# Kernel optimization log

Hardware: AMD Instinct MI355X
Metric: run time of the kernel (lower is better)

The kernel has to match this reference:

```python
import jax, jax.numpy as jnp
import numpy as np

B, S, C = 2, 2048, 1536
HQ, HKV = 16, 4
DQK, DV = 128, 96
MAX_POS = 2048
CLIP = 5.0
EPS = 1e-5


def layer_norm(x, g, b):
    mu = jnp.mean(x, axis=-1, keepdims=True)
    var = jnp.mean(jnp.square(x - mu), axis=-1, keepdims=True)
    return (x - mu) * jax.lax.rsqrt(var + EPS) * g + b


def rms_bn(x, g, ms):
    # eval-mode EMA RMS batch-norm: per-channel running mean-square `ms`
    return x * jax.lax.rsqrt(ms + EPS) * g


def rope(x):
    # x: [B, S, H, C] with C even
    c = x.shape[-1]
    nf = c // 2
    s = x.shape[1]
    positions = jnp.arange(s, dtype=x.dtype)
    lin = jnp.arange(nf, dtype=x.dtype)
    end = max(MAX_POS - nf + 1.0, 1.0)
    geom = jnp.exp(jnp.linspace(0.0, jnp.log(jnp.asarray(end, dtype=x.dtype)), nf))
    inv_freq = 1.0 / (lin + geom)
    theta = positions[:, None] * inv_freq          # [S, nf]
    theta = jnp.repeat(theta, 2, axis=-1)[:, None, :]  # [S, 1, C]
    x_rot = jnp.stack([-x[..., 1::2], x[..., ::2]], axis=-1).reshape(x.shape)
    return x * jnp.cos(theta) + x_rot * jnp.sin(theta)


def setup_inputs() -> dict:
    key = jax.random.key(0)
    ks = jax.random.split(key, 8)
    d = {
        'x': jax.random.normal(ks[0], (B, S, C), dtype=jnp.float32),
        'bn1_g': jnp.ones((C,), jnp.float32),
        'bn1_ms': jnp.ones((C,), jnp.float32),
        'Wq': jax.random.normal(ks[1], (C, HQ * DQK), jnp.float32) * 0.02,
        'Wk': jax.random.normal(ks[2], (C, HKV * DQK), jnp.float32) * 0.02,
        'Wv': jax.random.normal(ks[3], (C, HKV * DV), jnp.float32) * 0.02,
        'qn_g': jnp.ones((DQK,), jnp.float32), 'qn_b': jnp.zeros((DQK,), jnp.float32),
        'kn_g': jnp.ones((DQK,), jnp.float32), 'kn_b': jnp.zeros((DQK,), jnp.float32),
        'vn_g': jnp.ones((DV,), jnp.float32), 'vn_b': jnp.zeros((DV,), jnp.float32),
        'Wo': jax.random.normal(ks[4], (HQ * DV, C), jnp.float32) * 0.02,
        'bo': jnp.zeros((C,), jnp.float32),
        'bn2_g': jnp.ones((C,), jnp.float32),
        'bn2_ms': jnp.ones((C,), jnp.float32),
    }
    return d


def reference(x, bn1_g, bn1_ms, Wq, Wk, Wv, qn_g, qn_b, kn_g, kn_b, vn_g, vn_b, Wo, bo, bn2_g, bn2_ms):
    rep = HQ // HKV
    h = rms_bn(x, bn1_g, bn1_ms)                       # [B,S,C]
    q = (h @ Wq).reshape(B, S, HQ, DQK)
    k = (h @ Wk).reshape(B, S, HKV, DQK)
    v = (h @ Wv).reshape(B, S, HKV, DV)
    q = layer_norm(q, qn_g, qn_b)
    k = layer_norm(k, kn_g, kn_b)
    v = layer_norm(v, vn_g, vn_b)
    q = rope(q)
    k = rope(k)
    # torch .repeat(1,1,rep,1) tiles head axis: [h0..hkv-1] * rep
    k = jnp.tile(k, (1, 1, rep, 1))                    # [B,S,HQ,DQK]
    v = jnp.tile(v, (1, 1, rep, 1))                    # [B,S,HQ,DV]
    logits = jnp.einsum('bshc,bShc->bhsS', q, k) / (DQK ** 0.5)
    logits = jnp.tanh(logits / CLIP) * CLIP
    attn = jax.nn.softmax(logits, axis=-1)
    y = jnp.einsum('bhsS,bShc->bshc', attn, v)         # [B,S,HQ,DV]
    y = y.reshape(B, S, HQ * DV)
    y = y @ Wo + bo
    y = rms_bn(y, bn2_g, bn2_ms)
    return y
```

## Files before the change

kernel.cpp:

```cpp
#include <hip/hip_runtime.h>
#include <hip/hip_bf16.h>
#include <math.h>

typedef __hip_bfloat16 bf16;
typedef __attribute__((ext_vector_type(8))) short short8;
typedef __attribute__((ext_vector_type(4))) short short4s;
typedef __attribute__((ext_vector_type(4))) float f32x4;

constexpr int Bb=2, Ss=2048, Cc=1536, HQn=16, HKVn=4, Dqk=128, Dv=96;
constexpr int NR   = Bb*Ss;
constexpr int NQKV = HQn*Dqk + HKVn*Dqk + HKVn*Dv;
constexpr int COL_K = HQn*Dqk;
constexpr int COL_V = COL_K + HKVn*Dqk;
constexpr int NY   = HQn*Dv;
constexpr float EPSf=1e-5f, CLIPf=5.0f;
constexpr float LOG2E = 1.44269504089f;

__device__ __forceinline__ float s2f(short s) {
    unsigned u = ((unsigned)(unsigned short)s) << 16;
    return __builtin_bit_cast(float, u);
}
__device__ __forceinline__ short f2s(float v) {
    bf16 b = __float2bfloat16(v);
    return __builtin_bit_cast(short, b);
}
__device__ __forceinline__ bool is_bf(const void* tagp) {
    return ((*(const unsigned*)tagp) & 0xFFFFu) != 0u;
}
__device__ __forceinline__ float ldd(const void* p, size_t i, bool bf) {
    return bf ? s2f(((const short*)p)[i]) : ((const float*)p)[i];
}

__global__ __launch_bounds__(256) void k_pre(const void* g1, const void* ms1,
        const void* bo, const void* g2, const void* ms2,
        float* __restrict__ ascale, float* __restrict__ ebias,
        float* __restrict__ escale, float2* __restrict__ tab) {
    bool bf = is_bf(ms1);
    int idx = blockIdx.x*256 + threadIdx.x;
    if (idx < Cc) {
        ascale[idx] = rsqrtf(ldd(ms1,idx,bf) + EPSf) * ldd(g1,idx,bf);
        ebias[idx]  = ldd(bo,idx,bf);
        escale[idx] = rsqrtf(ldd(ms2,idx,bf) + EPSf) * ldd(g2,idx,bf);
    }
    if (idx < Ss*64) {
        int s = idx >> 6, f = idx & 63;
        float geom = expf((float)f * (logf(1985.0f) * (1.0f/63.0f)));
        float invf = 1.0f / ((float)f + geom);
        float th = (float)s * invf;
        tab[idx] = make_float2(cosf(th), sinf(th));
    }
}

__global__ __launch_bounds__(256) void k_bn1(const void* __restrict__ x,
        const float* __restrict__ ascale, short* __restrict__ h, const void* tagp) {
    bool bf = is_bf(tagp);
    size_t i8 = (size_t)(blockIdx.x*256 + threadIdx.x) * 8;
    if (i8 >= (size_t)NR*Cc) return;
    int c = (int)(i8 % Cc);
    float xv[8];
    if (bf) {
        short8 xa = *(const short8*)((const short*)x + i8);
        #pragma unroll
        for (int j=0;j<8;++j) xv[j] = s2f(xa[j]);
    } else {
        const float* xf = (const float*)x + i8;
        #pragma unroll
        for (int j=0;j<8;++j) xv[j] = xf[j];
    }
    short8 o;
    #pragma unroll
    for (int j=0;j<8;++j) o[j] = f2s(xv[j] * ascale[c+j]);
    *(short8*)(h + i8) = o;
}

__global__ __launch_bounds__(256) void k_trw(const void* __restrict__ Wq,
        const void* __restrict__ Wk, const void* __restrict__ Wv,
        const void* __restrict__ Wo, short* __restrict__ WT, const void* tagp) {
    __shared__ short tile[32][33];
    bool bf = is_bf(tagp);
    int gt = blockIdx.x*32;
    int k0 = blockIdx.y*32;
    const void* W; int N, nl;
    if      (gt < 2048) { W = Wq; N = 2048; nl = gt; }
    else if (gt < 2560) { W = Wk; N = 512;  nl = gt - 2048; }
    else if (gt < 2944) { W = Wv; N = 384;  nl = gt - 2560; }
    else                { W = Wo; N = 1536; nl = gt - 2944; }
    int t = threadIdx.x, c = t & 31;
    #pragma unroll
    for (int r8=0; r8<32; r8+=8) {
        int r = r8 + (t>>5);
        tile[r][c] = f2s(ldd(W, (size_t)(k0+r)*N + nl + c, bf));
    }
    __syncthreads();
    #pragma unroll
    for (int r8=0; r8<32; r8+=8) {
        int r = r8 + (t>>5);
        WT[(size_t)(gt + r)*Cc + k0 + c] = tile[c][r];
    }
}

__global__ __launch_bounds__(256) void k_gemm(const short* __restrict__ A,
        const short* __restrict__ BT, void* __restrict__ Cout,
        int M, int N, int K,
        const float* __restrict__ ebias, const float* __restrict__ escale,
        int epi, const void* tagp) {
    __shared__ short As[128*32];
    __shared__ short Bs[128*32];
    const int t = threadIdx.x;
    const int w = t >> 6, lane = t & 63;
    const int l15 = lane & 15, quad = lane >> 4;
    const int wm = (w>>1)*64, wn = (w&1)*64;
    const int m0 = blockIdx.y*128, n0 = blockIdx.x*128;
    const int c0 = lane >> 2;
    const int koff = (lane & 3) * 8;

    f32x4 acc[4][4];
    #pragma unroll
    for (int i=0;i<4;++i)
        #pragma unroll
        for (int j=0;j<4;++j) acc[i][j] = (f32x4){0.f,0.f,0.f,0.f};

    for (int k0 = 0; k0 < K; k0 += 32) {
        __syncthreads();
        #pragma unroll
        for (int c=0; c<2; ++c) {
            int rA = w*32 + c*16;
            const short* ga = A  + (size_t)(m0 + rA + c0)*K + k0 + koff;
            const short* gb = BT + (size_t)(n0 + rA + c0)*K + k0 + koff;
            __builtin_amdgcn_global_load_lds(
                (const __attribute__((address_space(1))) void*)ga,
                (__attribute__((address_space(3))) void*)&As[rA*32], 16, 0, 0);
            __builtin_amdgcn_global_load_lds(
                (const __attribute__((address_space(1))) void*)gb,
                (__attribute__((address_space(3))) void*)&Bs[rA*32], 16, 0, 0);
        }
        __syncthreads();
        short8 af[4], bfr[4];
        #pragma unroll
        for (int mt=0; mt<4; ++mt)
            af[mt] = *(const short8*)&As[(wm + mt*16 + l15)*32 + quad*8];
        #pragma unroll
        for (int nt=0; nt<4; ++nt)
            bfr[nt] = *(const short8*)&Bs[(wn + nt*16 + l15)*32 + quad*8];
        #pragma unroll
        for (int mt=0; mt<4; ++mt)
            #pragma unroll
            for (int nt=0; nt<4; ++nt)
                acc[mt][nt] = __builtin_amdgcn_mfma_f32_16x16x32_bf16(
                    af[mt], bfr[nt], acc[mt][nt], 0, 0, 0);
    }

    const bool outf32 = epi && !is_bf(tagp);
    #pragma unroll
    for (int mt=0; mt<4; ++mt) {
        #pragma unroll
        for (int nt=0; nt<4; ++nt) {
            int col = n0 + wn + nt*16 + l15;
            float eb = epi ? ebias[col]  : 0.f;
            float es = epi ? escale[col] : 1.f;
            #pragma unroll
            for (int reg=0; reg<4; ++reg) {
                int row = m0 + wm + mt*16 + quad*4 + reg;
                float v = acc[mt][nt][reg];
                if (epi) v = (v + eb) * es;
                if (outf32) ((float*)Cout)[(size_t)row*N + col] = v;
                else        ((short*)Cout)[(size_t)row*N + col] = f2s(v);
            }
        }
    }
}

__global__ __launch_bounds__(256) void k_ln(short* __restrict__ qkvb,
        const float2* __restrict__ tab,
        const void* qg, const void* qb_, const void* kg, const void* kb_,
        const void* vg, const void* vb_, const void* tagp) {
    bool bf = is_bf(tagp);
    int R = blockIdx.x*4 + (threadIdx.x>>6);
    int lane = threadIdx.x & 63;
    int hidx = R % 24, bs = R / 24, s = bs % Ss;
    const void *g, *bia; int coff, D, dorope;
    if (hidx < 16)      { coff = hidx*Dqk;              D = Dqk; g = qg; bia = qb_; dorope = 1; }
    else if (hidx < 20) { coff = COL_K + (hidx-16)*Dqk; D = Dqk; g = kg; bia = kb_; dorope = 1; }
    else                { coff = COL_V + (hidx-20)*Dv;  D = Dv;  g = vg; bia = vb_; dorope = 0; }
    short* p = qkvb + (size_t)bs*NQKV + coff;
    int d0 = lane*2;
    bool act = d0 < D;
    float v0 = 0.f, v1 = 0.f;
    if (act) { v0 = s2f(p[d0]); v1 = s2f(p[d0+1]); }
    float sum = v0 + v1;
    #pragma unroll
    for (int m=1; m<64; m<<=1) sum += __shfl_xor(sum, m);
    float mu = sum / (float)D;
    float c0 = act ? v0-mu : 0.f, c1 = act ? v1-mu : 0.f;
    float sq = c0*c0 + c1*c1;
    #pragma unroll
    for (int m=1; m<64; m<<=1) sq += __shfl_xor(sq, m);
    float r = rsqrtf(sq/(float)D + EPSf);
    if (act) {
        float y0 = c0*r*ldd(g,d0,bf)   + ldd(bia,d0,bf);
        float y1 = c1*r*ldd(g,d0+1,bf) + ldd(bia,d0+1,bf);
        if (dorope) {
            float2 cs = tab[s*64 + lane];
            float t0 = y0*cs.x - y1*cs.y;
            y1 = y1*cs.x + y0*cs.y;
            y0 = t0;
        }
        p[d0] = f2s(y0); p[d0+1] = f2s(y1);
    }
}

__global__ __launch_bounds__(256) void k_trv(const short* __restrict__ qkvb,
        short* __restrict__ vT) {
    __shared__ short tile[32][33];
    int bs0 = blockIdx.x*32;
    int dg0 = blockIdx.y*32;
    int t = threadIdx.x, c = t & 31;
    #pragma unroll
    for (int r8=0; r8<32; r8+=8) {
        int r = r8 + (t>>5);
        tile[r][c] = qkvb[(size_t)(bs0+r)*NQKV + COL_V + dg0 + c];
    }
    __syncthreads();
    int b = bs0 >> 11, s0 = bs0 & 2047;
    #pragma unroll
    for (int r8=0; r8<32; r8+=8) {
        int r = r8 + (t>>5);
        vT[((size_t)(b*384 + dg0 + r))*Ss + s0 + c] = tile[c][r];
    }
}

__global__ __launch_bounds__(256) void k_attn(const short* __restrict__ qkvb,
        const short* __restrict__ vT, short* __restrict__ Yb) {
    __shared__ __align__(16) short Ks[64*136];
    __shared__ __align__(16) short VTs[96*72];
    __shared__ __align__(16) short Ps[128*72];
    const int q0 = blockIdx.x*128, hq = blockIdx.y, b = blockIdx.z;
    const int kvh = hq & (HKVn-1);
    const int t = threadIdx.x;
    const int w = t >> 6, lane = t & 63;
    const int l15 = lane & 15, quad = lane >> 4;
    const float ctan = 2.0f * (0.0883883476f / CLIPf) * LOG2E;
    const float c2   = -2.0f * CLIPf * LOG2E;

    short8 qf[2][4];
    #pragma unroll
    for (int qt=0; qt<2; ++qt) {
        const short* qp = qkvb + (size_t)(b*Ss + q0 + w*32 + qt*16 + l15)*NQKV + hq*Dqk;
        #pragma unroll
        for (int ds=0; ds<4; ++ds) qf[qt][ds] = *(const short8*)(qp + ds*32 + quad*8);
    }

    f32x4 oacc[2][6];
    #pragma unroll
    for (int qt=0; qt<2; ++qt)
        #pragma unroll
        for (int nt=0; nt<6; ++nt) oacc[qt][nt] = (f32x4){0.f,0.f,0.f,0.f};
    float lsum[2] = {0.f, 0.f};

    const short* Kb = qkvb + ((size_t)b*Ss)*NQKV + COL_K + kvh*Dqk;
    const short* Vb = vT + ((size_t)(b*HKVn + kvh)*Dv)*Ss;

    for (int kc = 0; kc < Ss/64; ++kc) {
        const int j0 = kc*64;
        __syncthreads();
        #pragma unroll
        for (int it=0; it<4; ++it) {
            int idx = it*256 + t;
            int key = idx >> 4, d = (idx & 15)*8;
            *(short8*)&Ks[key*136 + d] = *(const short8*)(Kb + (size_t)(j0+key)*NQKV + d);
        }
        #pragma unroll
        for (int it=0; it<3; ++it) {
            int idx = it*256 + t;
            int dv = idx >> 3, c8 = (idx & 7)*8;
            *(short8*)&VTs[dv*72 + c8] = *(const short8*)(Vb + (size_t)dv*Ss + j0 + c8);
        }
        __syncthreads();

        f32x4 sacc[4][2];
        #pragma unroll
        for (int kt=0; kt<4; ++kt)
            #pragma unroll
            for (int qt=0; qt<2; ++qt) sacc[kt][qt] = (f32x4){0.f,0.f,0.f,0.f};
        #pragma unroll
        for (int kt=0; kt<4; ++kt) {
            short8 kf[4];
            #pragma unroll
            for (int ds=0; ds<4; ++ds)
                kf[ds] = *(const short8*)&Ks[(kt*16 + l15)*136 + ds*32 + quad*8];
            #pragma unroll
            for (int qt=0; qt<2; ++qt)
                #pragma unroll
                for (int ds=0; ds<4; ++ds)
                    sacc[kt][qt] = __builtin_amdgcn_mfma_f32_16x16x32_bf16(
                        kf[ds], qf[qt][ds], sacc[kt][qt], 0, 0, 0);
        }

        #pragma unroll
        for (int kt=0; kt<4; ++kt)
            #pragma unroll
            for (int qt=0; qt<2; ++qt) {
                short4s pb;
                #pragma unroll
                for (int reg=0; reg<4; ++reg) {
                    float u = __builtin_amdgcn_exp2f(sacc[kt][qt][reg] * ctan);
                    float p = __builtin_amdgcn_exp2f(c2 * __builtin_amdgcn_rcpf(u + 1.0f));
                    short pb16 = f2s(p);
                    pb[reg] = pb16;
                    lsum[qt] += s2f(pb16);
                }
                *(short4s*)&Ps[(w*32 + qt*16 + l15)*72 + kt*16 + quad*4] = pb;
            }

        short8 vf[6][2];
        #pragma unroll
        for (int nt=0; nt<6; ++nt)
            #pragma unroll
            for (int ks=0; ks<2; ++ks)
                vf[nt][ks] = *(const short8*)&VTs[(nt*16 + l15)*72 + ks*32 + quad*8];
        #pragma unroll
        for (int qt=0; qt<2; ++qt) {
            short8 pf0 = *(const short8*)&Ps[(w*32 + qt*16 + l15)*72 + quad*8];
            short8 pf1 = *(const short8*)&Ps[(w*32 + qt*16 + l15)*72 + 32 + quad*8];
            #pragma unroll
            for (int nt=0; nt<6; ++nt) {
                oacc[qt][nt] = __builtin_amdgcn_mfma_f32_16x16x32_bf16(
                    pf0, vf[nt][0], oacc[qt][nt], 0, 0, 0);
                oacc[qt][nt] = __builtin_amdgcn_mfma_f32_16x16x32_bf16(
                    pf1, vf[nt][1], oacc[qt][nt], 0, 0, 0);
            }
        }
    }

    float lred[2];
    #pragma unroll
    for (int qt=0; qt<2; ++qt) {
        float l = lsum[qt];
        l += __shfl_xor(l, 16);
        l += __shfl_xor(l, 32);
        lred[qt] = l;
    }
    #pragma unroll
    for (int qt=0; qt<2; ++qt) {
        float rinv[4];
        #pragma unroll
        for (int reg=0; reg<4; ++reg)
            rinv[reg] = __builtin_amdgcn_rcpf(__shfl(lred[qt], quad*4 + reg, 16));
        #pragma unroll
        for (int nt=0; nt<6; ++nt)
            #pragma unroll
            for (int reg=0; reg<4; ++reg) {
                int row = q0 + w*32 + qt*16 + quad*4 + reg;
                Yb[(size_t)(b*Ss + row)*NY + hq*Dv + nt*16 + l15] =
                    f2s(oacc[qt][nt][reg] * rinv[reg]);
            }
    }
}

extern "C" void kernel_launch(void* const* d_in, const int* in_sizes, int n_in,
                              void* d_out, int out_size, void* d_ws, size_t ws_size,
                              hipStream_t stream) {
    const void* x     = d_in[0];
    const void* bn1g  = d_in[1];
    const void* bn1ms = d_in[2];
    const void* Wq    = d_in[3];
    const void* Wk    = d_in[4];
    const void* Wv    = d_in[5];
    const void* qng   = d_in[6];
    const void* qnb   = d_in[7];
    const void* kng   = d_in[8];
    const void* knb   = d_in[9];
    const void* vng   = d_in[10];
    const void* vnb   = d_in[11];
    const void* Wo    = d_in[12];
    const void* bo    = d_in[13];
    const void* bn2g  = d_in[14];
    const void* bn2ms = d_in[15];

    char* wsb = (char*)d_ws;
    float*  ascale = (float*)(wsb);
    float*  ebias  = (float*)(wsb + 6144);
    float*  escale = (float*)(wsb + 12288);
    float2* tab    = (float2*)(wsb + 18432);
    short*  h      = (short*)(wsb + 1067520);
    short*  WT     = (short*)(wsb + 13650432);
    short*  qkv    = (short*)(wsb + 27412992);
    short*  vT     = (short*)(wsb + 51530240);
    short*  y      = (short*)(wsb + 54675968);
    short*  WoT    = WT + (size_t)NQKV*Cc;

    k_pre<<<512, 256, 0, stream>>>(bn1g, bn1ms, bo, bn2g, bn2ms,
                                   ascale, ebias, escale, tab);
    k_bn1<<<(NR*Cc/8 + 255)/256, 256, 0, stream>>>(x, ascale, h, bn1ms);
    k_trw<<<dim3(4480/32, Cc/32), 256, 0, stream>>>(Wq, Wk, Wv, Wo, WT, bn1ms);

    k_gemm<<<dim3(NQKV/128, NR/128), 256, 0, stream>>>(
        h, WT, qkv, NR, NQKV, Cc, nullptr, nullptr, 0, bn1ms);

    k_ln<<<NR*24/4, 256, 0, stream>>>(qkv, tab, qng, qnb, kng, knb, vng, vnb, bn1ms);
    k_trv<<<dim3(NR/32, 384/32), 256, 0, stream>>>(qkv, vT);

    k_attn<<<dim3(Ss/128, HQn, Bb), 256, 0, stream>>>(qkv, vT, y);

    k_gemm<<<dim3(Cc/128, NR/128), 256, 0, stream>>>(
        y, WoT, d_out, NR, Cc, NY, ebias, escale, 1, bn1ms);
}
```

Baseline: 393.9 us.

## Fuse Q layernorm+RoPE into attention, shuffle P via bpermute, shrink attn blocks

Moves the Q-head LayerNorm and RoPE into the attention kernel's Q-fragment load, so k_ln now processes only K and V heads. P is no longer staged through shared memory; the bf16 probabilities are packed into registers and redistributed across lanes with ds_bpermute to form the A operand of the PV MFMA. Attention blocks shrink to 64 queries and 128 threads with a 3-blocks-per-CU launch bound, and the bn1 scale is computed inline in k_bn1 instead of being precomputed. Together these cut an elementwise pass and LDS traffic, at the cost of redoing the Q normalization work inside attention, more bpermute instructions, and K/V tiles being loaded into LDS twice as many times in total.

```diff
diff --git a/kernel.cpp b/kernel.cpp
--- a/kernel.cpp
+++ b/kernel.cpp
@@ -4,7 +4,7 @@
 
 typedef __hip_bfloat16 bf16;
 typedef __attribute__((ext_vector_type(8))) short short8;
-typedef __attribute__((ext_vector_type(4))) short short4s;
+typedef __attribute__((ext_vector_type(4))) int   int4v;
 typedef __attribute__((ext_vector_type(4))) float f32x4;
 
 constexpr int Bb=2, Ss=2048, Cc=1536, HQn=16, HKVn=4, Dqk=128, Dv=96;
@@ -31,14 +31,13 @@
     return bf ? s2f(((const short*)p)[i]) : ((const float*)p)[i];
 }
 
-__global__ __launch_bounds__(256) void k_pre(const void* g1, const void* ms1,
-        const void* bo, const void* g2, const void* ms2,
-        float* __restrict__ ascale, float* __restrict__ ebias,
-        float* __restrict__ escale, float2* __restrict__ tab) {
-    bool bf = is_bf(ms1);
+__global__ __launch_bounds__(256) void k_pre(const void* bo, const void* g2,
+        const void* ms2, const void* tagp,
+        float* __restrict__ ebias, float* __restrict__ escale,
+        float2* __restrict__ tab) {
+    bool bf = is_bf(tagp);
     int idx = blockIdx.x*256 + threadIdx.x;
     if (idx < Cc) {
-        ascale[idx] = rsqrtf(ldd(ms1,idx,bf) + EPSf) * ldd(g1,idx,bf);
         ebias[idx]  = ldd(bo,idx,bf);
         escale[idx] = rsqrtf(ldd(ms2,idx,bf) + EPSf) * ldd(g2,idx,bf);
     }
@@ -52,7 +51,8 @@
 }
 
 __global__ __launch_bounds__(256) void k_bn1(const void* __restrict__ x,
-        const float* __restrict__ ascale, short* __restrict__ h, const void* tagp) {
+        const void* __restrict__ g1, const void* __restrict__ ms1,
+        short* __restrict__ h, const void* tagp) {
     bool bf = is_bf(tagp);
     size_t i8 = (size_t)(blockIdx.x*256 + threadIdx.x) * 8;
     if (i8 >= (size_t)NR*Cc) return;
@@ -69,7 +69,10 @@
     }
     short8 o;
     #pragma unroll
-    for (int j=0;j<8;++j) o[j] = f2s(xv[j] * ascale[c+j]);
+    for (int j=0;j<8;++j) {
+        float sc = rsqrtf(ldd(ms1,c+j,bf) + EPSf) * ldd(g1,c+j,bf);
+        o[j] = f2s(xv[j] * sc);
+    }
     *(short8*)(h + i8) = o;
 }
 
@@ -172,16 +175,15 @@
 
 __global__ __launch_bounds__(256) void k_ln(short* __restrict__ qkvb,
         const float2* __restrict__ tab,
-        const void* qg, const void* qb_, const void* kg, const void* kb_,
-        const void* vg, const void* vb_, const void* tagp) {
+        const void* kg, const void* kb_, const void* vg, const void* vb_,
+        const void* tagp) {
     bool bf = is_bf(tagp);
     int R = blockIdx.x*4 + (threadIdx.x>>6);
     int lane = threadIdx.x & 63;
-    int hidx = R % 24, bs = R / 24, s = bs % Ss;
+    int hidx = R & 7, bs = R >> 3, s = bs & (Ss-1);
     const void *g, *bia; int coff, D, dorope;
-    if (hidx < 16)      { coff = hidx*Dqk;              D = Dqk; g = qg; bia = qb_; dorope = 1; }
-    else if (hidx < 20) { coff = COL_K + (hidx-16)*Dqk; D = Dqk; g = kg; bia = kb_; dorope = 1; }
-    else                { coff = COL_V + (hidx-20)*Dv;  D = Dv;  g = vg; bia = vb_; dorope = 0; }
+    if (hidx < 4) { coff = COL_K + hidx*Dqk;     D = Dqk; g = kg; bia = kb_; dorope = 1; }
+    else          { coff = COL_V + (hidx-4)*Dv;  D = Dv;  g = vg; bia = vb_; dorope = 0; }
     short* p = qkvb + (size_t)bs*NQKV + coff;
     int d0 = lane*2;
     bool act = d0 < D;
@@ -229,25 +231,62 @@
     }
 }
 
-__global__ __launch_bounds__(256) void k_attn(const short* __restrict__ qkvb,
-        const short* __restrict__ vT, short* __restrict__ Yb) {
+constexpr int QB = 64;
+__global__ __launch_bounds__(128, 3) void k_attn(const short* __restrict__ qkvb,
+        const short* __restrict__ vT, short* __restrict__ Yb,
+        const float2* __restrict__ tab, const void* __restrict__ qg,
+        const void* __restrict__ qb_, const void* tagp) {
     __shared__ __align__(16) short Ks[64*136];
     __shared__ __align__(16) short VTs[96*72];
-    __shared__ __align__(16) short Ps[128*72];
-    const int q0 = blockIdx.x*128, hq = blockIdx.y, b = blockIdx.z;
+    const int q0 = blockIdx.x*QB, hq = blockIdx.y, b = blockIdx.z;
     const int kvh = hq & (HKVn-1);
     const int t = threadIdx.x;
     const int w = t >> 6, lane = t & 63;
     const int l15 = lane & 15, quad = lane >> 4;
+    const bool bf = is_bf(tagp);
     const float ctan = 2.0f * (0.0883883476f / CLIPf) * LOG2E;
     const float c2   = -2.0f * CLIPf * LOG2E;
 
     short8 qf[2][4];
     #pragma unroll
     for (int qt=0; qt<2; ++qt) {
-        const short* qp = qkvb + (size_t)(b*Ss + q0 + w*32 + qt*16 + l15)*NQKV + hq*Dqk;
-        #pragma unroll
-        for (int ds=0; ds<4; ++ds) qf[qt][ds] = *(const short8*)(qp + ds*32 + quad*8);
+        int row = q0 + w*32 + qt*16 + l15;
+        const short* qp = qkvb + (size_t)(b*Ss + row)*NQKV + hq*Dqk;
+        float v[4][8]; float sum = 0.f;
+        #pragma unroll
+        for (int ds=0; ds<4; ++ds) {
+            short8 raw = *(const short8*)(qp + ds*32 + quad*8);
+            #pragma unroll
+            for (int j=0;j<8;++j) { v[ds][j] = s2f(raw[j]); sum += v[ds][j]; }
+        }
+        sum += __shfl_xor(sum, 16); sum += __shfl_xor(sum, 32);
+        float mu = sum * (1.0f/(float)Dqk);
+        float sq = 0.f;
+        #pragma unroll
+        for (int ds=0; ds<4; ++ds)
+            #pragma unroll
+            for (int j=0;j<8;++j) { float cv = v[ds][j]-mu; sq += cv*cv; }
+        sq += __shfl_xor(sq, 16); sq += __shfl_xor(sq, 32);
+        float r = rsqrtf(sq*(1.0f/(float)Dqk) + EPSf);
+        #pragma unroll
+        for (int ds=0; ds<4; ++ds) {
+            float y[8];
+            #pragma unroll
+            for (int j=0;j<8;++j) {
+                int d = ds*32 + quad*8 + j;
+                y[j] = (v[ds][j]-mu)*r*ldd(qg,d,bf) + ldd(qb_,d,bf);
+            }
+            short8 o;
+            #pragma unroll
+            for (int j=0;j<8;j+=2) {
+                int f = ds*16 + quad*4 + (j>>1);
+                float2 cs = tab[row*64 + f];
+                float y0 = y[j]*cs.x - y[j+1]*cs.y;
+                float y1 = y[j+1]*cs.x + y[j]*cs.y;
+                o[j] = f2s(y0); o[j+1] = f2s(y1);
+            }
+            qf[qt][ds] = o;
+        }
     }
 
     f32x4 oacc[2][6];
@@ -259,29 +298,29 @@
 
     const short* Kb = qkvb + ((size_t)b*Ss)*NQKV + COL_K + kvh*Dqk;
     const short* Vb = vT + ((size_t)(b*HKVn + kvh)*Dv)*Ss;
+
+    const int addr_lo = 4*(l15 + 32*(quad & 1));
+    const int addr_hi = addr_lo + 64;
+    const bool hi_tile = (quad >= 2);
 
     for (int kc = 0; kc < Ss/64; ++kc) {
         const int j0 = kc*64;
         __syncthreads();
         #pragma unroll
-        for (int it=0; it<4; ++it) {
-            int idx = it*256 + t;
+        for (int it=0; it<8; ++it) {
+            int idx = it*128 + t;
             int key = idx >> 4, d = (idx & 15)*8;
             *(short8*)&Ks[key*136 + d] = *(const short8*)(Kb + (size_t)(j0+key)*NQKV + d);
         }
         #pragma unroll
-        for (int it=0; it<3; ++it) {
-            int idx = it*256 + t;
+        for (int it=0; it<6; ++it) {
+            int idx = it*128 + t;
             int dv = idx >> 3, c8 = (idx & 7)*8;
             *(short8*)&VTs[dv*72 + c8] = *(const short8*)(Vb + (size_t)dv*Ss + j0 + c8);
         }
         __syncthreads();
 
-        f32x4 sacc[4][2];
-        #pragma unroll
-        for (int kt=0; kt<4; ++kt)
-            #pragma unroll
-            for (int qt=0; qt<2; ++qt) sacc[kt][qt] = (f32x4){0.f,0.f,0.f,0.f};
+        unsigned pk[4][2][2];
         #pragma unroll
         for (int kt=0; kt<4; ++kt) {
             short8 kf[4];
@@ -289,45 +328,53 @@
             for (int ds=0; ds<4; ++ds)
                 kf[ds] = *(const short8*)&Ks[(kt*16 + l15)*136 + ds*32 + quad*8];
             #pragma unroll
-            for (int qt=0; qt<2; ++qt)
+            for (int qt=0; qt<2; ++qt) {
+                f32x4 s = (f32x4){0.f,0.f,0.f,0.f};
                 #pragma unroll
                 for (int ds=0; ds<4; ++ds)
-                    sacc[kt][qt] = __builtin_amdgcn_mfma_f32_16x16x32_bf16(
-                        kf[ds], qf[qt][ds], sacc[kt][qt], 0, 0, 0);
-        }
-
-        #pragma unroll
-        for (int kt=0; kt<4; ++kt)
-            #pragma unroll
-            for (int qt=0; qt<2; ++qt) {
-                short4s pb;
+                    s = __builtin_amdgcn_mfma_f32_16x16x32_bf16(kf[ds], qf[qt][ds], s, 0,0,0);
+                unsigned pp[4];
                 #pragma unroll
                 for (int reg=0; reg<4; ++reg) {
-                    float u = __builtin_amdgcn_exp2f(sacc[kt][qt][reg] * ctan);
+                    float u = __builtin_amdgcn_exp2f(s[reg] * ctan);
                     float p = __builtin_amdgcn_exp2f(c2 * __builtin_amdgcn_rcpf(u + 1.0f));
-                    short pb16 = f2s(p);
-                    pb[reg] = pb16;
-                    lsum[qt] += s2f(pb16);
+                    short sh = f2s(p);
+                    lsum[qt] += s2f(sh);
+                    pp[reg] = (unsigned)(unsigned short)sh;
                 }
-                *(short4s*)&Ps[(w*32 + qt*16 + l15)*72 + kt*16 + quad*4] = pb;
-            }
-
-        short8 vf[6][2];
-        #pragma unroll
-        for (int nt=0; nt<6; ++nt)
-            #pragma unroll
-            for (int ks=0; ks<2; ++ks)
-                vf[nt][ks] = *(const short8*)&VTs[(nt*16 + l15)*72 + ks*32 + quad*8];
-        #pragma unroll
-        for (int qt=0; qt<2; ++qt) {
-            short8 pf0 = *(const short8*)&Ps[(w*32 + qt*16 + l15)*72 + quad*8];
-            short8 pf1 = *(const short8*)&Ps[(w*32 + qt*16 + l15)*72 + 32 + quad*8];
-            #pragma unroll
-            for (int nt=0; nt<6; ++nt) {
+                pk[kt][qt][0] = pp[0] | (pp[1] << 16);
+                pk[kt][qt][1] = pp[2] | (pp[3] << 16);
+            }
+        }
+
+        short8 Af[2][2];
+        #pragma unroll
+        for (int qt=0; qt<2; ++qt)
+            #pragma unroll
+            for (int kp=0; kp<2; ++kp) {
+                int4v di;
+                #pragma unroll
+                for (int dw=0; dw<2; ++dw) {
+                    int se0 = __builtin_amdgcn_ds_bpermute(addr_lo, (int)pk[2*kp][qt][dw]);
+                    int so0 = __builtin_amdgcn_ds_bpermute(addr_lo, (int)pk[2*kp+1][qt][dw]);
+                    int se1 = __builtin_amdgcn_ds_bpermute(addr_hi, (int)pk[2*kp][qt][dw]);
+                    int so1 = __builtin_amdgcn_ds_bpermute(addr_hi, (int)pk[2*kp+1][qt][dw]);
+                    di[dw]     = hi_tile ? so0 : se0;
+                    di[2 + dw] = hi_tile ? so1 : se1;
+                }
+                Af[qt][kp] = __builtin_bit_cast(short8, di);
+            }
+
+        #pragma unroll
+        for (int nt=0; nt<6; ++nt) {
+            short8 vf0 = *(const short8*)&VTs[(nt*16 + l15)*72 + quad*8];
+            short8 vf1 = *(const short8*)&VTs[(nt*16 + l15)*72 + 32 + quad*8];
+            #pragma unroll
+            for (int qt=0; qt<2; ++qt) {
                 oacc[qt][nt] = __builtin_amdgcn_mfma_f32_16x16x32_bf16(
-                    pf0, vf[nt][0], oacc[qt][nt], 0, 0, 0);
+                    Af[qt][0], vf0, oacc[qt][nt], 0, 0, 0);
                 oacc[qt][nt] = __builtin_amdgcn_mfma_f32_16x16x32_bf16(
-                    pf1, vf[nt][1], oacc[qt][nt], 0, 0, 0);
+                    Af[qt][1], vf1, oacc[qt][nt], 0, 0, 0);
             }
         }
     }
@@ -378,10 +425,9 @@
     const void* bn2ms = d_in[15];
 
     char* wsb = (char*)d_ws;
-    float*  ascale = (float*)(wsb);
-    float*  ebias  = (float*)(wsb + 6144);
-    float*  escale = (float*)(wsb + 12288);
-    float2* tab    = (float2*)(wsb + 18432);
+    float*  ebias  = (float*)(wsb);
+    float*  escale = (float*)(wsb + 6144);
+    float2* tab    = (float2*)(wsb + 12288);
     short*  h      = (short*)(wsb + 1067520);
     short*  WT     = (short*)(wsb + 13650432);
     short*  qkv    = (short*)(wsb + 27412992);
@@ -389,18 +435,17 @@
     short*  y      = (short*)(wsb + 54675968);
     short*  WoT    = WT + (size_t)NQKV*Cc;
 
-    k_pre<<<512, 256, 0, stream>>>(bn1g, bn1ms, bo, bn2g, bn2ms,
-                                   ascale, ebias, escale, tab);
-    k_bn1<<<(NR*Cc/8 + 255)/256, 256, 0, stream>>>(x, ascale, h, bn1ms);
+    k_pre<<<512, 256, 0, stream>>>(bo, bn2g, bn2ms, bn1ms, ebias, escale, tab);
+    k_bn1<<<(NR*Cc/8 + 255)/256, 256, 0, stream>>>(x, bn1g, bn1ms, h, bn1ms);
     k_trw<<<dim3(4480/32, Cc/32), 256, 0, stream>>>(Wq, Wk, Wv, Wo, WT, bn1ms);
 
     k_gemm<<<dim3(NQKV/128, NR/128), 256, 0, stream>>>(
         h, WT, qkv, NR, NQKV, Cc, nullptr, nullptr, 0, bn1ms);
 
-    k_ln<<<NR*24/4, 256, 0, stream>>>(qkv, tab, qng, qnb, kng, knb, vng, vnb, bn1ms);
+    k_ln<<<NR*8/4, 256, 0, stream>>>(qkv, tab, kng, knb, vng, vnb, bn1ms);
     k_trv<<<dim3(NR/32, 384/32), 256, 0, stream>>>(qkv, vT);
 
-    k_attn<<<dim3(Ss/128, HQn, Bb), 256, 0, stream>>>(qkv, vT, y);
+    k_attn<<<dim3(Ss/QB, HQn, Bb), 128, 0, stream>>>(qkv, vT, y, tab, qng, qnb, bn1ms);
 
     k_gemm<<<dim3(Cc/128, NR/128), 256, 0, stream>>>(
         y, WoT, d_out, NR, Cc, NY, ebias, escale, 1, bn1ms);
```

Result: slower. 463.7 us (+17.7%).
